# Performance work log

Measured on AMD Instinct MI355X. Metric: run time of the kernel, lower is better.

Reference implementation:

```python
import jax, jax.numpy as jnp
import numpy as np

B, H, W, C = 64, 56, 56, 96
HEADS, WIN, SHIFT = 3, 7, 3
HD = C // HEADS          # head dim = 32
MLP_H = 4 * C            # mlp_ratio = 4
NW = (H // WIN) * (W // WIN)  # 64 windows per image
WW = WIN * WIN           # 49 tokens per window


def _rel_index():
    ch, cw = np.meshgrid(np.arange(WIN), np.arange(WIN), indexing='ij')
    coords = np.stack([ch, cw]).reshape(2, -1)            # [2, 49]
    rel = (coords[:, :, None] - coords[:, None, :]).transpose(1, 2, 0)
    rel[..., 0] += WIN - 1
    rel[..., 1] += WIN - 1
    rel[..., 0] *= 2 * WIN - 1
    return rel.sum(-1)                                    # [49, 49] int

REL_IDX = _rel_index()


def _attn_mask():
    # shifted-window mask per the original Swin implementation
    img = np.zeros((H, W))
    cnt = 0
    for hs in (slice(0, -WIN), slice(-WIN, -SHIFT), slice(-SHIFT, None)):
        for ws in (slice(0, -WIN), slice(-WIN, -SHIFT), slice(-SHIFT, None)):
            img[hs, ws] = cnt
            cnt += 1
    mw = img.reshape(H // WIN, WIN, W // WIN, WIN).transpose(0, 2, 1, 3).reshape(-1, WW)
    m = mw[:, None, :] - mw[:, :, None]
    return np.where(m != 0, -100.0, 0.0).astype(np.float32)  # [NW, 49, 49]

ATTN_MASK = jnp.asarray(_attn_mask())


def window_partition(x):
    # [B, H, W, C] -> [B*NW, 49, C]
    x = x.reshape(-1, H // WIN, WIN, W // WIN, WIN, C)
    return x.transpose(0, 1, 3, 2, 4, 5).reshape(-1, WW, C)


def window_reverse(w):
    # [B*NW, 49, C] -> [B, H, W, C]
    w = w.reshape(-1, H // WIN, W // WIN, WIN, WIN, C)
    return w.transpose(0, 1, 3, 2, 4, 5).reshape(-1, H, W, C)


def layernorm(x, w, b):
    mu = x.mean(-1, keepdims=True)
    var = ((x - mu) ** 2).mean(-1, keepdims=True)
    return (x - mu) / jnp.sqrt(var + 1e-5) * w + b


def setup_inputs() -> dict:
    key = jax.random.key(0)
    ks = jax.random.split(key, 16)
    s = 0.02
    return {
        'x': jax.random.normal(ks[0], (B, H * W, C), jnp.float32),
        'norm1_w': jnp.ones((C,), jnp.float32),
        'norm1_b': jnp.zeros((C,), jnp.float32),
        'qkv_w': jax.random.normal(ks[1], (3 * C, C), jnp.float32) * s,
        'qkv_b': jnp.zeros((3 * C,), jnp.float32),
        'rel_bias': jax.random.normal(ks[2], ((2 * WIN - 1) ** 2, HEADS), jnp.float32) * s,
        'proj_w': jax.random.normal(ks[3], (C, C), jnp.float32) * s,
        'proj_b': jnp.zeros((C,), jnp.float32),
        'norm2_w': jnp.ones((C,), jnp.float32),
        'norm2_b': jnp.zeros((C,), jnp.float32),
        'fc1_w': jax.random.normal(ks[4], (MLP_H, C), jnp.float32) * s,
        'fc1_b': jnp.zeros((MLP_H,), jnp.float32),
        'fc2_w': jax.random.normal(ks[5], (C, MLP_H), jnp.float32) * s,
        'fc2_b': jnp.zeros((C,), jnp.float32),
    }


def reference(x, norm1_w, norm1_b, qkv_w, qkv_b, rel_bias, proj_w, proj_b,
              norm2_w, norm2_b, fc1_w, fc1_b, fc2_w, fc2_b):
    shortcut = x
    h = layernorm(x, norm1_w, norm1_b).reshape(B, H, W, C)
    # cyclic shift (SW-MSA)
    h = jnp.roll(h, (-SHIFT, -SHIFT), axis=(1, 2))
    xw = window_partition(h)                               # [B*NW, 49, C]
    qkv = (xw @ qkv_w.T + qkv_b).reshape(-1, WW, 3, HEADS, HD)
    qkv = qkv.transpose(2, 0, 3, 1, 4)                     # [3, B*NW, heads, 49, hd]
    q, k, v = qkv[0], qkv[1], qkv[2]
    attn = jnp.einsum('whqd,whkd->whqk', q * (HD ** -0.5), k)   # [B*NW, heads, 49, 49]
    attn = attn + rel_bias[REL_IDX].transpose(2, 0, 1)[None]
    attn = attn.reshape(B, NW, HEADS, WW, WW) + ATTN_MASK[None, :, None]
    attn = jax.nn.softmax(attn.reshape(-1, HEADS, WW, WW), axis=-1)
    out = jnp.einsum('whqk,whkd->whqd', attn, v)
    out = out.transpose(0, 2, 1, 3).reshape(-1, WW, C)
    out = out @ proj_w.T + proj_b
    h = window_reverse(out)
    h = jnp.roll(h, (SHIFT, SHIFT), axis=(1, 2)).reshape(B, H * W, C)
    x = shortcut + h
    h2 = layernorm(x, norm2_w, norm2_b)
    h2 = jax.nn.gelu(h2 @ fc1_w.T + fc1_b, approximate=False) @ fc2_w.T + fc2_b
    return x + h2
```

## Files before the change

### kernel.cpp

```cpp
#include <hip/hip_runtime.h>
#include <hip/hip_bf16.h>
#include <math.h>

#define BATCH 64
#define HH 56
#define CH 96
#define HEADS 3
#define WIN 7
#define SHIFT 3
#define TOK 49
#define MLPH 384
#define SCALE 0.17677669529663687f

typedef short bf16x8 __attribute__((ext_vector_type(8)));
typedef float f32x4 __attribute__((ext_vector_type(4)));

#define MFMA(a, b, c) __builtin_amdgcn_mfma_f32_16x16x32_bf16((a), (b), (c), 0, 0, 0)
#define MEMFENCE() asm volatile("" ::: "memory")

__device__ __forceinline__ bf16x8 ldfrag(const __hip_bfloat16* p) {
    return *(const bf16x8*)p;
}
__device__ __forceinline__ unsigned short f2bf(float f) {
    __hip_bfloat16 h = __float2bfloat16(f);
    unsigned short u; __builtin_memcpy(&u, &h, 2); return u;
}

__global__ __launch_bounds__(256) void prep(
    const float* __restrict__ qkvw, const float* __restrict__ projw,
    const float* __restrict__ fc1w, const float* __restrict__ fc2w,
    const float* __restrict__ relb,
    __hip_bfloat16* __restrict__ wbf, float* __restrict__ btab)
{
    int i = blockIdx.x * 256 + threadIdx.x;
    if (i < 27648)        wbf[i] = __float2bfloat16(qkvw[i]);
    else if (i < 36864)   wbf[i] = __float2bfloat16(projw[i - 27648]);
    else if (i < 73728)   wbf[i] = __float2bfloat16(fc1w[i - 36864]);
    else if (i < 110592)  wbf[i] = __float2bfloat16(fc2w[i - 73728]);
    else {
        int j = i - 110592;
        int cat = j / 12288;
        int r = j - cat * 12288;
        int h = r >> 12;
        int r2 = r & 4095;
        int q = r2 >> 6, k = r2 & 63;
        float v;
        if (k >= TOK) v = -10000.f;
        else if (q >= TOK) v = 0.f;
        else {
            int qi = q / WIN, qj = q - qi * WIN;
            int ki = k / WIN, kj = k - ki * WIN;
            int ridx = (qi - ki + 6) * 13 + (qj - kj + 6);
            v = relb[ridx * HEADS + h];
            int rqh = (cat & 2) ? (qi < 4 ? 1 : 2) : 0;
            int rqw = (cat & 1) ? (qj < 4 ? 1 : 2) : 0;
            int rkh = (cat & 2) ? (ki < 4 ? 1 : 2) : 0;
            int rkw = (cat & 1) ? (kj < 4 ? 1 : 2) : 0;
            if (rqh * 3 + rqw != rkh * 3 + rkw) v -= 100.f;
        }
        btab[j] = v;
    }
}

__global__ __launch_bounds__(256) void swin_attn(
    const float* __restrict__ x,
    const float* __restrict__ n1w, const float* __restrict__ n1b,
    const __hip_bfloat16* __restrict__ wqkv, const float* __restrict__ qkvb,
    const float* __restrict__ btab,
    const __hip_bfloat16* __restrict__ wproj, const float* __restrict__ projb,
    float* __restrict__ out)
{
    __shared__ __align__(16) __hip_bfloat16 XL[64][104];
    __shared__ __align__(16) __hip_bfloat16 Qf[64][104];
    __shared__ __align__(16) __hip_bfloat16 Kf[64][104];
    __shared__ __align__(16) __hip_bfloat16 Vt[96][72];
    __shared__ __align__(16) __hip_bfloat16 Pw[4][16][72];

    const int blk = blockIdx.x;
    const int b = blk >> 6, win = blk & 63;
    const int wi = win >> 3, wj = win & 7;
    const int cat = ((wi == 7) << 1) | (wj == 7);
    const int tid = threadIdx.x;
    const int lane = tid & 63, w = tid >> 6;
    const int lr = lane & 15, g = lane >> 4;
    const int k0 = g * 8;
    const size_t bbase = (size_t)b * (HH * HH * CH);

    {
        int r = tid >> 2, p = tid & 3;
        if (r < TOK) {
            int ti = r / WIN, tj = r - (r / WIN) * WIN;
            int ph = wi * WIN + ti + SHIFT; if (ph >= HH) ph -= HH;
            int pw = wj * WIN + tj + SHIFT; if (pw >= HH) pw -= HH;
            const float4* xr = (const float4*)(x + bbase + (size_t)(ph * HH + pw) * CH + p * 24);
            float v[24]; float s = 0.f, s2 = 0.f;
            #pragma unroll
            for (int i = 0; i < 6; ++i) {
                float4 f = xr[i];
                v[4*i] = f.x; v[4*i+1] = f.y; v[4*i+2] = f.z; v[4*i+3] = f.w;
            }
            #pragma unroll
            for (int i = 0; i < 24; ++i) { s += v[i]; s2 += v[i] * v[i]; }
            s  += __shfl_xor(s, 1);  s  += __shfl_xor(s, 2);
            s2 += __shfl_xor(s2, 1); s2 += __shfl_xor(s2, 2);
            float mu = s * (1.f / CH);
            float rstd = rsqrtf(s2 * (1.f / CH) - mu * mu + 1e-5f);
            #pragma unroll
            for (int i = 0; i < 24; ++i) {
                int c = p * 24 + i;
                XL[r][c] = __float2bfloat16((v[i] - mu) * rstd * n1w[c] + n1b[c]);
            }
        } else {
            #pragma unroll
            for (int i = 0; i < 24; ++i) XL[r][p * 24 + i] = __float2bfloat16(0.f);
        }
    }
    __syncthreads();

    {
        bf16x8 Bx[4][3];
        #pragma unroll
        for (int tt = 0; tt < 4; ++tt)
            #pragma unroll
            for (int ks = 0; ks < 3; ++ks)
                Bx[tt][ks] = ldfrag(&XL[tt * 16 + lr][ks * 32 + k0]);
        #pragma unroll
        for (int nn = 0; nn < 5; ++nn) {
            int n = w + 4 * nn;
            if (n < 18) {
                const __hip_bfloat16* wp = wqkv + (n * 16 + lr) * CH + k0;
                bf16x8 Af[3];
                #pragma unroll
                for (int ks = 0; ks < 3; ++ks) Af[ks] = ldfrag(wp + ks * 32);
                f32x4 acc[4];
                #pragma unroll
                for (int tt = 0; tt < 4; ++tt) acc[tt] = (f32x4){0.f, 0.f, 0.f, 0.f};
                #pragma unroll
                for (int ks = 0; ks < 3; ++ks)
                    #pragma unroll
                    for (int tt = 0; tt < 4; ++tt)
                        acc[tt] = MFMA(Af[ks], Bx[tt][ks], acc[tt]);
                f32x4 b4 = *(const f32x4*)(qkvb + n * 16 + 4 * g);
                #pragma unroll
                for (int tt = 0; tt < 4; ++tt) {
                    int tokr = tt * 16 + lr;
                    if (n < 6) {
                        ushort4 u;
                        u.x = f2bf((acc[tt][0] + b4[0]) * SCALE);
                        u.y = f2bf((acc[tt][1] + b4[1]) * SCALE);
                        u.z = f2bf((acc[tt][2] + b4[2]) * SCALE);
                        u.w = f2bf((acc[tt][3] + b4[3]) * SCALE);
                        *(ushort4*)&Qf[tokr][n * 16 + 4 * g] = u;
                    } else if (n < 12) {
                        ushort4 u;
                        u.x = f2bf(acc[tt][0] + b4[0]);
                        u.y = f2bf(acc[tt][1] + b4[1]);
                        u.z = f2bf(acc[tt][2] + b4[2]);
                        u.w = f2bf(acc[tt][3] + b4[3]);
                        *(ushort4*)&Kf[tokr][(n - 6) * 16 + 4 * g] = u;
                    } else {
                        #pragma unroll
                        for (int j = 0; j < 4; ++j)
                            Vt[(n - 12) * 16 + 4 * g + j][tokr] =
                                __float2bfloat16(acc[tt][j] + b4[j]);
                    }
                }
            }
        }
    }
    __syncthreads();

    for (int u = w; u < 12; u += 4) {
        int h = u >> 2, qt = u & 3;
        bf16x8 qfrag = ldfrag(&Qf[qt * 16 + lr][h * 32 + k0]);
        f32x4 s[4];
        #pragma unroll
        for (int kt = 0; kt < 4; ++kt) {
            f32x4 z = {0.f, 0.f, 0.f, 0.f};
            s[kt] = MFMA(ldfrag(&Kf[kt * 16 + lr][h * 32 + k0]), qfrag, z);
        }
        const float* bt = btab + (((cat * HEADS + h) << 12) | ((qt * 16 + lr) << 6));
        #pragma unroll
        for (int kt = 0; kt < 4; ++kt)
            s[kt] += *(const f32x4*)(bt + kt * 16 + 4 * g);
        float m = -1e30f;
        #pragma unroll
        for (int kt = 0; kt < 4; ++kt)
            #pragma unroll
            for (int j = 0; j < 4; ++j) m = fmaxf(m, s[kt][j]);
        m = fmaxf(m, __shfl_xor(m, 16));
        m = fmaxf(m, __shfl_xor(m, 32));
        float e[4][4]; float sum = 0.f;
        #pragma unroll
        for (int kt = 0; kt < 4; ++kt)
            #pragma unroll
            for (int j = 0; j < 4; ++j) { e[kt][j] = __expf(s[kt][j] - m); sum += e[kt][j]; }
        sum += __shfl_xor(sum, 16);
        sum += __shfl_xor(sum, 32);
        float inv = 1.f / sum;
        #pragma unroll
        for (int kt = 0; kt < 4; ++kt) {
            ushort2 p0, p1;
            p0.x = f2bf(e[kt][0] * inv); p0.y = f2bf(e[kt][1] * inv);
            p1.x = f2bf(e[kt][2] * inv); p1.y = f2bf(e[kt][3] * inv);
            *(ushort2*)&Pw[w][lr][kt * 16 + g * 4]     = p0;
            *(ushort2*)&Pw[w][lr][kt * 16 + g * 4 + 2] = p1;
        }
        MEMFENCE();
        #pragma unroll
        for (int dt = 0; dt < 2; ++dt) {
            f32x4 o = {0.f, 0.f, 0.f, 0.f};
            #pragma unroll
            for (int ks = 0; ks < 2; ++ks) {
                bf16x8 pa = ldfrag(&Pw[w][lr][ks * 32 + k0]);
                bf16x8 vb = ldfrag(&Vt[h * 32 + dt * 16 + lr][ks * 32 + k0]);
                o = MFMA(pa, vb, o);
            }
            #pragma unroll
            for (int j = 0; j < 4; ++j)
                XL[qt * 16 + g * 4 + j][h * 32 + dt * 16 + lr] = __float2bfloat16(o[j]);
        }
    }
    __syncthreads();

    {
        bf16x8 Bx[4][3];
        #pragma unroll
        for (int tt = 0; tt < 4; ++tt)
            #pragma unroll
            for (int ks = 0; ks < 3; ++ks)
                Bx[tt][ks] = ldfrag(&XL[tt * 16 + lr][ks * 32 + k0]);
        #pragma unroll
        for (int nn = 0; nn < 2; ++nn) {
            int n = w + 4 * nn;
            if (n < 6) {
                const __hip_bfloat16* wp = wproj + (n * 16 + lr) * CH + k0;
                bf16x8 Af[3];
                #pragma unroll
                for (int ks = 0; ks < 3; ++ks) Af[ks] = ldfrag(wp + ks * 32);
                f32x4 acc[4];
                #pragma unroll
                for (int tt = 0; tt < 4; ++tt) acc[tt] = (f32x4){0.f, 0.f, 0.f, 0.f};
                #pragma unroll
                for (int ks = 0; ks < 3; ++ks)
                    #pragma unroll
                    for (int tt = 0; tt < 4; ++tt)
                        acc[tt] = MFMA(Af[ks], Bx[tt][ks], acc[tt]);
                f32x4 b4 = *(const f32x4*)(projb + n * 16 + 4 * g);
                #pragma unroll
                for (int tt = 0; tt < 4; ++tt) {
                    int tokr = tt * 16 + lr;
                    if (tokr < TOK) {
                        int ti = tokr / WIN, tj = tokr - (tokr / WIN) * WIN;
                        int ph = wi * WIN + ti + SHIFT; if (ph >= HH) ph -= HH;
                        int pw = wj * WIN + tj + SHIFT; if (pw >= HH) pw -= HH;
                        size_t gi = bbase + (size_t)(ph * HH + pw) * CH + n * 16 + 4 * g;
                        f32x4 x4 = *(const f32x4*)(x + gi);
                        *(f32x4*)(out + gi) = x4 + acc[tt] + b4;
                    }
                }
            }
        }
    }
}

__global__ __launch_bounds__(256) void swin_mlp(
    float* __restrict__ out,
    const float* __restrict__ n2w, const float* __restrict__ n2b,
    const __hip_bfloat16* __restrict__ w1, const float* __restrict__ b1,
    const __hip_bfloat16* __restrict__ w2, const float* __restrict__ b2)
{
    __shared__ __align__(16) __hip_bfloat16 XL2[64][104];
    __shared__ __align__(16) __hip_bfloat16 Hs[64][204];

    const int tid = threadIdx.x;
    const int lane = tid & 63, w = tid >> 6;
    const int lr = lane & 15, g = lane >> 4, k0 = g * 8;
    const size_t base = (size_t)blockIdx.x * 64 * CH;

    {
        int r = tid >> 2, p = tid & 3;
        const float4* xr = (const float4*)(out + base + (size_t)r * CH + p * 24);
        float v[24]; float s = 0.f, s2 = 0.f;
        #pragma unroll
        for (int i = 0; i < 6; ++i) {
            float4 f = xr[i];
            v[4*i] = f.x; v[4*i+1] = f.y; v[4*i+2] = f.z; v[4*i+3] = f.w;
        }
        #pragma unroll
        for (int i = 0; i < 24; ++i) { s += v[i]; s2 += v[i] * v[i]; }
        s  += __shfl_xor(s, 1);  s  += __shfl_xor(s, 2);
        s2 += __shfl_xor(s2, 1); s2 += __shfl_xor(s2, 2);
        float mu = s * (1.f / CH);
        float rstd = rsqrtf(s2 * (1.f / CH) - mu * mu + 1e-5f);
        #pragma unroll
        for (int i = 0; i < 6; ++i) {
            const float* wp4 = n2w + p * 24 + 4 * i;
            const float* bp4 = n2b + p * 24 + 4 * i;
            ushort4 u;
            u.x = f2bf((v[4*i]   - mu) * rstd * wp4[0] + bp4[0]);
            u.y = f2bf((v[4*i+1] - mu) * rstd * wp4[1] + bp4[1]);
            u.z = f2bf((v[4*i+2] - mu) * rstd * wp4[2] + bp4[2]);
            u.w = f2bf((v[4*i+3] - mu) * rstd * wp4[3] + bp4[3]);
            *(ushort4*)&XL2[r][p * 24 + 4 * i] = u;
        }
    }
    __syncthreads();

    const int mh = w & 1, nh = w >> 1;
    f32x4 acc2[3][2];
    #pragma unroll
    for (int nt = 0; nt < 3; ++nt)
        #pragma unroll
        for (int mi = 0; mi < 2; ++mi) acc2[nt][mi] = (f32x4){0.f, 0.f, 0.f, 0.f};

    #pragma unroll
    for (int c = 0; c < 2; ++c) {
        bf16x8 Bx[4][3];
        #pragma unroll
        for (int tt = 0; tt < 4; ++tt)
            #pragma unroll
            for (int ks = 0; ks < 3; ++ks)
                Bx[tt][ks] = ldfrag(&XL2[tt * 16 + lr][ks * 32 + k0]);

        #pragma unroll
        for (int nn = 0; nn < 3; ++nn) {
            int nl = w + 4 * nn;
            int ncol = c * 192 + nl * 16;
            const __hip_bfloat16* wp = w1 + (ncol + lr) * CH + k0;
            bf16x8 Af[3];
            #pragma unroll
            for (int ks = 0; ks < 3; ++ks) Af[ks] = ldfrag(wp + ks * 32);
            f32x4 acc[4];
            #pragma unroll
            for (int tt = 0; tt < 4; ++tt) acc[tt] = (f32x4){0.f, 0.f, 0.f, 0.f};
            #pragma unroll
            for (int ks = 0; ks < 3; ++ks)
                #pragma unroll
                for (int tt = 0; tt < 4; ++tt)
                    acc[tt] = MFMA(Af[ks], Bx[tt][ks], acc[tt]);
            f32x4 b4 = *(const f32x4*)(b1 + ncol + 4 * g);
            #pragma unroll
            for (int tt = 0; tt < 4; ++tt) {
                ushort4 u;
                #pragma unroll
                for (int j = 0; j < 4; ++j) {
                    float v = acc[tt][j] + b4[j];
                    float ge = v / (1.f + __expf(-1.702f * v));
                    ((unsigned short*)&u)[j] = f2bf(ge);
                }
                *(ushort4*)&Hs[tt * 16 + lr][nl * 16 + 4 * g] = u;
            }
        }
        __syncthreads();

        #pragma unroll
        for (int k = 0; k < 6; ++k) {
            bf16x8 h0 = ldfrag(&Hs[mh * 32 + lr][k * 32 + k0]);
            bf16x8 h1 = ldfrag(&Hs[mh * 32 + 16 + lr][k * 32 + k0]);
            #pragma unroll
            for (int nt = 0; nt < 3; ++nt) {
                bf16x8 Af = ldfrag(w2 + (nh * 48 + nt * 16 + lr) * MLPH + c * 192 + k * 32 + k0);
                acc2[nt][0] = MFMA(Af, h0, acc2[nt][0]);
                acc2[nt][1] = MFMA(Af, h1, acc2[nt][1]);
            }
        }
        __syncthreads();
    }

    #pragma unroll
    for (int nt = 0; nt < 3; ++nt) {
        f32x4 b4 = *(const f32x4*)(b2 + nh * 48 + nt * 16 + 4 * g);
        #pragma unroll
        for (int mi = 0; mi < 2; ++mi) {
            int tok = mh * 32 + mi * 16 + lr;
            size_t gi = base + (size_t)tok * CH + nh * 48 + nt * 16 + 4 * g;
            f32x4 r4 = *(const f32x4*)(out + gi);
            *(f32x4*)(out + gi) = r4 + acc2[nt][mi] + b4;
        }
    }
}

extern "C" void kernel_launch(void* const* d_in, const int* in_sizes, int n_in,
                              void* d_out, int out_size, void* d_ws, size_t ws_size,
                              hipStream_t stream) {
    const float* x     = (const float*)d_in[0];
    const float* n1w   = (const float*)d_in[1];
    const float* n1b   = (const float*)d_in[2];
    const float* qkvw  = (const float*)d_in[3];
    const float* qkvb  = (const float*)d_in[4];
    const float* relb  = (const float*)d_in[5];
    const float* projw = (const float*)d_in[6];
    const float* projb = (const float*)d_in[7];
    const float* n2w   = (const float*)d_in[8];
    const float* n2b   = (const float*)d_in[9];
    const float* fc1w  = (const float*)d_in[10];
    const float* fc1b  = (const float*)d_in[11];
    const float* fc2w  = (const float*)d_in[12];
    const float* fc2b  = (const float*)d_in[13];
    float* out = (float*)d_out;

    __hip_bfloat16* wbf = (__hip_bfloat16*)d_ws;
    float* btab = (float*)((char*)d_ws + 221184);
    const __hip_bfloat16* wqkv  = wbf;
    const __hip_bfloat16* wproj = wbf + 27648;
    const __hip_bfloat16* wfc1  = wbf + 36864;
    const __hip_bfloat16* wfc2  = wbf + 73728;

    prep<<<624, 256, 0, stream>>>(qkvw, projw, fc1w, fc2w, relb, wbf, btab);
    swin_attn<<<BATCH * 64, 256, 0, stream>>>(
        x, n1w, n1b, wqkv, qkvb, btab, wproj, projb, out);
    swin_mlp<<<(BATCH * HH * HH) / 64, 256, 0, stream>>>(
        out, n2w, n2b, wfc1, fc1b, wfc2, fc2b);
}
```

Baseline: 206.0 us.

## Fuse window attention and MLP into a single per-window kernel

```diff
diff --git a/kernel.cpp b/kernel.cpp
--- a/kernel.cpp
+++ b/kernel.cpp
@@ -62,19 +62,25 @@
     }
 }
 
-__global__ __launch_bounds__(256) void swin_attn(
+__global__ __launch_bounds__(256) void swin_fused(
     const float* __restrict__ x,
     const float* __restrict__ n1w, const float* __restrict__ n1b,
     const __hip_bfloat16* __restrict__ wqkv, const float* __restrict__ qkvb,
     const float* __restrict__ btab,
     const __hip_bfloat16* __restrict__ wproj, const float* __restrict__ projb,
+    const float* __restrict__ n2w, const float* __restrict__ n2b,
+    const __hip_bfloat16* __restrict__ w1, const float* __restrict__ b1,
+    const __hip_bfloat16* __restrict__ w2, const float* __restrict__ b2,
     float* __restrict__ out)
 {
-    __shared__ __align__(16) __hip_bfloat16 XL[64][104];
-    __shared__ __align__(16) __hip_bfloat16 Qf[64][104];
-    __shared__ __align__(16) __hip_bfloat16 Kf[64][104];
-    __shared__ __align__(16) __hip_bfloat16 Vt[96][72];
-    __shared__ __align__(16) __hip_bfloat16 Pw[4][16][72];
+    __shared__ __align__(16) char arena[65536];
+    auto XL   = (__hip_bfloat16(*)[104])(arena);
+    auto Qf   = (__hip_bfloat16(*)[104])(arena + 13312);
+    auto Kf   = (__hip_bfloat16(*)[104])(arena + 26624);
+    auto Vt   = (__hip_bfloat16(*)[72])(arena + 39936);
+    auto Pw   = (__hip_bfloat16(*)[16][72])(arena + 53760);
+    auto resL = (float(*)[104])(arena + 13312);
+    auto Hs   = (__hip_bfloat16(*)[200])(arena + 39936);
 
     const int blk = blockIdx.x;
     const int b = blk >> 6, win = blk & 63;
@@ -256,36 +262,23 @@
                         int pw = wj * WIN + tj + SHIFT; if (pw >= HH) pw -= HH;
                         size_t gi = bbase + (size_t)(ph * HH + pw) * CH + n * 16 + 4 * g;
                         f32x4 x4 = *(const f32x4*)(x + gi);
-                        *(f32x4*)(out + gi) = x4 + acc[tt] + b4;
+                        *(f32x4*)&resL[tokr][n * 16 + 4 * g] = x4 + acc[tt] + b4;
+                    } else {
+                        *(f32x4*)&resL[tokr][n * 16 + 4 * g] = (f32x4){0.f, 0.f, 0.f, 0.f};
                     }
                 }
             }
         }
     }
-}
-
-__global__ __launch_bounds__(256) void swin_mlp(
-    float* __restrict__ out,
-    const float* __restrict__ n2w, const float* __restrict__ n2b,
-    const __hip_bfloat16* __restrict__ w1, const float* __restrict__ b1,
-    const __hip_bfloat16* __restrict__ w2, const float* __restrict__ b2)
-{
-    __shared__ __align__(16) __hip_bfloat16 XL2[64][104];
-    __shared__ __align__(16) __hip_bfloat16 Hs[64][204];
-
-    const int tid = threadIdx.x;
-    const int lane = tid & 63, w = tid >> 6;
-    const int lr = lane & 15, g = lane >> 4, k0 = g * 8;
-    const size_t base = (size_t)blockIdx.x * 64 * CH;
+    __syncthreads();
 
     {
         int r = tid >> 2, p = tid & 3;
-        const float4* xr = (const float4*)(out + base + (size_t)r * CH + p * 24);
         float v[24]; float s = 0.f, s2 = 0.f;
         #pragma unroll
         for (int i = 0; i < 6; ++i) {
-            float4 f = xr[i];
-            v[4*i] = f.x; v[4*i+1] = f.y; v[4*i+2] = f.z; v[4*i+3] = f.w;
+            f32x4 f = *(const f32x4*)&resL[r][p * 24 + 4 * i];
+            v[4*i] = f[0]; v[4*i+1] = f[1]; v[4*i+2] = f[2]; v[4*i+3] = f[3];
         }
         #pragma unroll
         for (int i = 0; i < 24; ++i) { s += v[i]; s2 += v[i] * v[i]; }
@@ -302,7 +295,7 @@
             u.y = f2bf((v[4*i+1] - mu) * rstd * wp4[1] + bp4[1]);
             u.z = f2bf((v[4*i+2] - mu) * rstd * wp4[2] + bp4[2]);
             u.w = f2bf((v[4*i+3] - mu) * rstd * wp4[3] + bp4[3]);
-            *(ushort4*)&XL2[r][p * 24 + 4 * i] = u;
+            *(ushort4*)&XL[r][p * 24 + 4 * i] = u;
         }
     }
     __syncthreads();
@@ -321,7 +314,7 @@
         for (int tt = 0; tt < 4; ++tt)
             #pragma unroll
             for (int ks = 0; ks < 3; ++ks)
-                Bx[tt][ks] = ldfrag(&XL2[tt * 16 + lr][ks * 32 + k0]);
+                Bx[tt][ks] = ldfrag(&XL[tt * 16 + lr][ks * 32 + k0]);
 
         #pragma unroll
         for (int nn = 0; nn < 3; ++nn) {
@@ -373,10 +366,15 @@
         f32x4 b4 = *(const f32x4*)(b2 + nh * 48 + nt * 16 + 4 * g);
         #pragma unroll
         for (int mi = 0; mi < 2; ++mi) {
-            int tok = mh * 32 + mi * 16 + lr;
-            size_t gi = base + (size_t)tok * CH + nh * 48 + nt * 16 + 4 * g;
-            f32x4 r4 = *(const f32x4*)(out + gi);
-            *(f32x4*)(out + gi) = r4 + acc2[nt][mi] + b4;
+            int tokr = mh * 32 + mi * 16 + lr;
+            if (tokr < TOK) {
+                int ti = tokr / WIN, tj = tokr - (tokr / WIN) * WIN;
+                int ph = wi * WIN + ti + SHIFT; if (ph >= HH) ph -= HH;
+                int pw = wj * WIN + tj + SHIFT; if (pw >= HH) pw -= HH;
+                size_t gi = bbase + (size_t)(ph * HH + pw) * CH + nh * 48 + nt * 16 + 4 * g;
+                f32x4 r4 = *(const f32x4*)&resL[tokr][nh * 48 + nt * 16 + 4 * g];
+                *(f32x4*)(out + gi) = r4 + acc2[nt][mi] + b4;
+            }
         }
     }
 }
@@ -408,8 +406,7 @@
     const __hip_bfloat16* wfc2  = wbf + 73728;
 
     prep<<<624, 256, 0, stream>>>(qkvw, projw, fc1w, fc2w, relb, wbf, btab);
-    swin_attn<<<BATCH * 64, 256, 0, stream>>>(
-        x, n1w, n1b, wqkv, qkvb, btab, wproj, projb, out);
-    swin_mlp<<<(BATCH * HH * HH) / 64, 256, 0, stream>>>(
-        out, n2w, n2b, wfc1, fc1b, wfc2, fc2b);
+    swin_fused<<<BATCH * 64, 256, 0, stream>>>(
+        x, n1w, n1b, wqkv, qkvb, btab, wproj, projb,
+        n2w, n2b, wfc1, fc1b, wfc2, fc2b, out);
 }
```

Result: slower. 219.4 us (+6.5%).
